# Kernel optimization log

Measured on AMD Instinct MI355X. Metric: run time of the kernel, lower is better.

## Reference

```python
import jax, jax.numpy as jnp
import numpy as np

NUM_INPUTS = 4096
NUM_LEAVES = 2048
BATCH = 16384


def setup_inputs() -> dict:
    key = jax.random.key(0)
    kx, ka = jax.random.split(key)
    x = jax.random.normal(kx, (BATCH, NUM_INPUTS), dtype=jnp.float32)
    hard_assignment = jax.random.randint(ka, (NUM_LEAVES,), 0, NUM_INPUTS, dtype=jnp.int64)
    return {"x": x, "hard_assignment": hard_assignment}


def reference(x, hard_assignment):
    # torch: x @ P_hard.T where P_hard[leaf, hard_assignment[leaf]] = 1.
    # A one-hot selection matmul is exactly a column gather of x:
    # out[b, leaf] = x[b, hard_assignment[leaf]]
    return jnp.take(x, hard_assignment, axis=1)  # [BATCH, NUM_LEAVES]
```

## Files before the change

### kernel.cpp

```cpp
#include <hip/hip_runtime.h>

#define NUM_INPUTS 4096
#define NUM_LEAVES 2048

__global__ __launch_bounds__(256) void FrozenInputToLeaf_gather(
    const float* __restrict__ x,
    const int* __restrict__ idx,
    float* __restrict__ out) {
    __shared__ float row[NUM_INPUTS];

    const int b = blockIdx.x;
    const int t = threadIdx.x;

    const float4* __restrict__ xv = (const float4*)(x + (size_t)b * NUM_INPUTS);
    float4* rv = (float4*)row;
#pragma unroll
    for (int j = 0; j < 4; ++j) {
        rv[t + j * 256] = xv[t + j * 256];
    }
    __syncthreads();

    const int4* __restrict__ iv = (const int4*)idx;
    const int4 i0 = iv[t * 2 + 0];
    const int4 i1 = iv[t * 2 + 1];

    float4 o0, o1;
    o0.x = row[i0.x];
    o0.y = row[i0.y];
    o0.z = row[i0.z];
    o0.w = row[i0.w];
    o1.x = row[i1.x];
    o1.y = row[i1.y];
    o1.z = row[i1.z];
    o1.w = row[i1.w];

    float4* __restrict__ ov = (float4*)(out + (size_t)b * NUM_LEAVES);
    ov[t * 2 + 0] = o0;
    ov[t * 2 + 1] = o1;
}

extern "C" void kernel_launch(void* const* d_in, const int* in_sizes, int n_in,
                              void* d_out, int out_size, void* d_ws, size_t ws_size,
                              hipStream_t stream) {
    const float* x = (const float*)d_in[0];
    const int* idx = (const int*)d_in[1];
    float* out = (float*)d_out;

    const int batch = in_sizes[0] / NUM_INPUTS;

    FrozenInputToLeaf_gather<<<batch, 256, 0, stream>>>(x, idx, out);
}
```

Baseline: 74.90 us.

## Use direct global-to-LDS loads and process two rows per block

Replaces register-staged row copies with global_load_lds direct-to-LDS transfers and has each block gather two batch rows, reusing the loaded index vectors. This aims to cut register/VGPR traffic and instruction count, and to amortize the index loads and per-block overhead. It doubles LDS per block, which may reduce occupancy, and relies on support for 16-byte global_load_lds.

```diff
diff --git a/kernel.cpp b/kernel.cpp
--- a/kernel.cpp
+++ b/kernel.cpp
@@ -2,41 +2,53 @@
 
 #define NUM_INPUTS 4096
 #define NUM_LEAVES 2048
+#define ROWS_PER_BLOCK 2
+#define BLK 256
 
-__global__ __launch_bounds__(256) void FrozenInputToLeaf_gather(
+typedef const __attribute__((address_space(1))) void* gas_ptr;
+typedef __attribute__((address_space(3))) void* las_ptr;
+
+__global__ __launch_bounds__(BLK) void FrozenInputToLeaf_gather2(
     const float* __restrict__ x,
     const int* __restrict__ idx,
     float* __restrict__ out) {
-    __shared__ float row[NUM_INPUTS];
+    __shared__ float rows[ROWS_PER_BLOCK][NUM_INPUTS];
 
-    const int b = blockIdx.x;
     const int t = threadIdx.x;
-
-    const float4* __restrict__ xv = (const float4*)(x + (size_t)b * NUM_INPUTS);
-    float4* rv = (float4*)row;
-#pragma unroll
-    for (int j = 0; j < 4; ++j) {
-        rv[t + j * 256] = xv[t + j * 256];
-    }
-    __syncthreads();
+    const size_t b0 = (size_t)blockIdx.x * ROWS_PER_BLOCK;
 
     const int4* __restrict__ iv = (const int4*)idx;
     const int4 i0 = iv[t * 2 + 0];
     const int4 i1 = iv[t * 2 + 1];
 
-    float4 o0, o1;
-    o0.x = row[i0.x];
-    o0.y = row[i0.y];
-    o0.z = row[i0.z];
-    o0.w = row[i0.w];
-    o1.x = row[i1.x];
-    o1.y = row[i1.y];
-    o1.z = row[i1.z];
-    o1.w = row[i1.w];
+#pragma unroll
+    for (int r = 0; r < ROWS_PER_BLOCK; ++r) {
+        const float* __restrict__ src = x + (b0 + r) * NUM_INPUTS;
+#pragma unroll
+        for (int j = 0; j < 4; ++j) {
+            const int e = (j * BLK + threadIdx.x) * 4;
+            __builtin_amdgcn_global_load_lds((gas_ptr)(src + e),
+                                             (las_ptr)(&rows[r][e]), 16, 0, 0);
+        }
+    }
+    __syncthreads();
 
-    float4* __restrict__ ov = (float4*)(out + (size_t)b * NUM_LEAVES);
-    ov[t * 2 + 0] = o0;
-    ov[t * 2 + 1] = o1;
+#pragma unroll
+    for (int r = 0; r < ROWS_PER_BLOCK; ++r) {
+        float4 o0, o1;
+        o0.x = rows[r][i0.x];
+        o0.y = rows[r][i0.y];
+        o0.z = rows[r][i0.z];
+        o0.w = rows[r][i0.w];
+        o1.x = rows[r][i1.x];
+        o1.y = rows[r][i1.y];
+        o1.z = rows[r][i1.z];
+        o1.w = rows[r][i1.w];
+
+        float4* __restrict__ ov = (float4*)(out + (b0 + r) * NUM_LEAVES);
+        ov[t * 2 + 0] = o0;
+        ov[t * 2 + 1] = o1;
+    }
 }
 
 extern "C" void kernel_launch(void* const* d_in, const int* in_sizes, int n_in,
@@ -47,6 +59,7 @@
     float* out = (float*)d_out;
 
     const int batch = in_sizes[0] / NUM_INPUTS;
+    const int grid = batch / ROWS_PER_BLOCK;
 
-    FrozenInputToLeaf_gather<<<batch, 256, 0, stream>>>(x, idx, out);
+    FrozenInputToLeaf_gather2<<<grid, BLK, 0, stream>>>(x, idx, out);
 }
```

After: 74.48 us. Within noise of the previous version (-0.6%).

## Gather directly from global memory instead of staging rows in LDS

Applied to the files above, without the earlier changes.

Drops the shared-memory staging of each input row and has each thread load its two selected elements straight from global memory. Block size grows to 1024 threads with float2 stores. This removes the LDS copy and barrier but relies on caches to merge scattered, uncoalesced loads, which risks redundant line fetches and lower effective bandwidth.

```diff
diff --git a/kernel.cpp b/kernel.cpp
--- a/kernel.cpp
+++ b/kernel.cpp
@@ -2,41 +2,25 @@
 
 #define NUM_INPUTS 4096
 #define NUM_LEAVES 2048
+#define BLK 1024
 
-__global__ __launch_bounds__(256) void FrozenInputToLeaf_gather(
+__global__ __launch_bounds__(BLK) void FrozenInputToLeaf_direct(
     const float* __restrict__ x,
     const int* __restrict__ idx,
     float* __restrict__ out) {
-    __shared__ float row[NUM_INPUTS];
+    const int t = threadIdx.x;
+    const size_t b = blockIdx.x;
 
-    const int b = blockIdx.x;
-    const int t = threadIdx.x;
+    const int2 i2 = ((const int2*)idx)[t];
 
-    const float4* __restrict__ xv = (const float4*)(x + (size_t)b * NUM_INPUTS);
-    float4* rv = (float4*)row;
-#pragma unroll
-    for (int j = 0; j < 4; ++j) {
-        rv[t + j * 256] = xv[t + j * 256];
-    }
-    __syncthreads();
+    const float* __restrict__ row = x + b * NUM_INPUTS;
 
-    const int4* __restrict__ iv = (const int4*)idx;
-    const int4 i0 = iv[t * 2 + 0];
-    const int4 i1 = iv[t * 2 + 1];
+    float2 v;
+    v.x = row[i2.x];
+    v.y = row[i2.y];
 
-    float4 o0, o1;
-    o0.x = row[i0.x];
-    o0.y = row[i0.y];
-    o0.z = row[i0.z];
-    o0.w = row[i0.w];
-    o1.x = row[i1.x];
-    o1.y = row[i1.y];
-    o1.z = row[i1.z];
-    o1.w = row[i1.w];
-
-    float4* __restrict__ ov = (float4*)(out + (size_t)b * NUM_LEAVES);
-    ov[t * 2 + 0] = o0;
-    ov[t * 2 + 1] = o1;
+    float2* __restrict__ ov = (float2*)(out + b * NUM_LEAVES);
+    ov[t] = v;
 }
 
 extern "C" void kernel_launch(void* const* d_in, const int* in_sizes, int n_in,
@@ -48,5 +32,5 @@
 
     const int batch = in_sizes[0] / NUM_INPUTS;
 
-    FrozenInputToLeaf_gather<<<batch, 256, 0, stream>>>(x, idx, out);
+    FrozenInputToLeaf_direct<<<batch, BLK, 0, stream>>>(x, idx, out);
 }
```

Result: slower. 81.24 us (+8.5%).
